# Optimization experiments

Hardware: AMD Instinct MI355X
Metric: run time of the kernel (lower is better)

The kernel has to match this reference:

```python
import jax, jax.numpy as jnp
import numpy as np

FIELD_NUM = 24

def _pair_indices(f):
    ii, jj = np.triu_indices(f, k=1)
    return jnp.asarray(ii), jnp.asarray(jj)

def setup_inputs() -> dict:
    key = jax.random.key(0)
    k1, k2 = jax.random.split(key)
    B, F, D = 16384, FIELD_NUM, 64
    P = F * (F - 1) // 2  # 276
    x = jax.random.normal(k1, (B, F, D), dtype=jnp.float32)
    W = jax.random.normal(k2, (P, D, D), dtype=jnp.float32) * 0.05
    return {"x": x, "W": W}

def reference(x, W):
    # x: (B, F, D) field embeddings; W: (P, D, D) per-pair bilinear matrices
    idx_i, idx_j = _pair_indices(FIELD_NUM)
    xi = x[:, idx_i, :]  # (B, P, D)
    xj = x[:, idx_j, :]  # (B, P, D)
    # sum_{p,d,e} xi[b,p,d] * W[p,d,e] * xj[b,p,e]
    logit = jnp.einsum('bpd,pde,bpe->b', xi, W, xj)
    return logit[:, None]  # (B, 1), matching tf output shape
```

## Files before the change

### kernel.cpp

```cpp
#include <hip/hip_runtime.h>
#include <stdint.h>

#define B_TOT 16384
#define F_NUM 24
#define D_DIM 64
#define P_NUM 276
#define BT    64
#define NTH   512
#define ROWS  770

typedef float f32x16 __attribute__((ext_vector_type(16)));
typedef short bf16x8 __attribute__((ext_vector_type(8)));

__device__ inline unsigned short f2bf(float f) {
    unsigned u = __float_as_uint(f);
    u += 0x7fffu + ((u >> 16) & 1u);
    return (unsigned short)(u >> 16);
}

struct WTab { int ent[8][36]; };
constexpr WTab build_tab() {
    WTab t{};
    const int fl[8][6] = {
        {0,12,-1,-1,-1,-1},
        {1,11,-1,-1,-1,-1},
        {2,10,-1,-1,-1,-1},
        {3, 9,-1,-1,-1,-1},
        {4, 8,-1,-1,-1,-1},
        {5, 7,-1,-1,-1,-1},
        {6,14,17,20,22,-1},
        {13,15,16,18,19,21}};
    for (int w = 0; w < 8; ++w) {
        int c = 0;
        for (int k = 0; k < 6; ++k) {
            int f = fl[w][k];
            if (f < 0) break;
            int base = 23 * f - f * (f - 1) / 2;
            for (int j = f + 1; j < 24; ++j)
                t.ent[w][c++] = (base + j - f - 1) | (j << 9) | (f << 14);
        }
        int last = t.ent[w][c - 1];
        while (c < 36) t.ent[w][c++] = last;
    }
    return t;
}
__device__ __constant__ WTab gtab = build_tab();

__global__ __launch_bounds__(256) void wprep(const float* __restrict__ W,
                                             unsigned short* __restrict__ afrag) {
    __shared__ __align__(16) unsigned short wlds[64 * 72];
    int p = blockIdx.x, t = threadIdx.x;
    const float4* src = (const float4*)(W + (size_t)p * 4096);
    #pragma unroll
    for (int c = 0; c < 4; ++c) {
        int i = t + c * 256;
        float4 v = src[i];
        int d = i >> 4;
        int e = (i & 15) * 4;
        ushort4 h; h.x=f2bf(v.x); h.y=f2bf(v.y); h.z=f2bf(v.z); h.w=f2bf(v.w);
        *(ushort4*)(&wlds[d * 72 + e]) = h;
    }
    __syncthreads();
    #pragma unroll
    for (int c = 0; c < 2; ++c) {
        int sl = t + c * 256;
        int u = sl >> 6, lane = sl & 63;
        int ks = u >> 1, m = u & 1;
        int d = m * 32 + (lane & 31);
        int e = ks * 16 + (lane >> 5) * 8;
        bf16x8 v = *(const bf16x8*)(&wlds[d * 72 + e]);
        size_t dst = ((size_t)((ks * P_NUM + p) * 2 + m) * 64 + lane) * 8;
        *(bf16x8*)(afrag + dst) = v;
    }
}

__global__ __launch_bounds__(NTH, 2) void fmfm_main(const float* __restrict__ x,
                                                    const unsigned short* __restrict__ afrag,
                                                    float* __restrict__ out) {
    __shared__ __align__(16) unsigned short xs[BT * ROWS];
    __shared__ float t_red[BT];
    const int tid = threadIdx.x;
    const int btile = blockIdx.x;
    const int lane = tid & 63;
    const int wv = __builtin_amdgcn_readfirstlane(tid >> 6);
    const int bcol = lane & 31;
    const int q = lane >> 5;

    if (tid < BT) t_red[tid] = 0.0f;

    const int cnt = (wv < 6) ? 34 : 36;
    const bf16x8* afr = (const bf16x8*)afrag;

    float tacc0 = 0.0f, tacc1 = 0.0f;
    f32x16 acc00, acc01, acc10, acc11;
    #pragma unroll
    for (int i = 0; i < 16; ++i) { acc00[i]=0.f; acc01[i]=0.f; acc10[i]=0.f; acc11[i]=0.f; }

    const float* xg  = x + (size_t)btile * BT * 1536;
    const float* xe0 = xg + (size_t)bcol * 1536 + 4 * q;
    const float* xe1 = xe0 + (size_t)32 * 1536;
    const unsigned short* xr0 = xs + bcol * ROWS;
    const unsigned short* xr1 = xs + (bcol + 32) * ROWS;

    for (int h = 0; h < 2; ++h) {
        __syncthreads();
        for (int k = 0; k < 24; ++k) {
            int g = tid + k * NTH;
            int row = g / 192;
            int r = g - row * 192;
            int f = r >> 3, i = r & 7;
            float4 v = *(const float4*)(xg + (size_t)row * 1536 + f * 64 + h * 32 + i * 4);
            ushort4 hh; hh.x=f2bf(v.x); hh.y=f2bf(v.y); hh.z=f2bf(v.z); hh.w=f2bf(v.w);
            *(ushort4*)(&xs[row * ROWS + f * 32 + i * 4]) = hh;
        }
        __syncthreads();

        const int ks0 = 2 * h;

        auto epi = [&](int f) {
            const float* e0 = xe0 + f * 64;
            const float* e1 = xe1 + f * 64;
            #pragma unroll
            for (int g = 0; g < 4; ++g) {
                float4 v = *(const float4*)(e0 + 8 * g);
                tacc0 += acc00[4*g+0]*v.x + acc00[4*g+1]*v.y + acc00[4*g+2]*v.z + acc00[4*g+3]*v.w;
                v = *(const float4*)(e0 + 32 + 8 * g);
                tacc0 += acc01[4*g+0]*v.x + acc01[4*g+1]*v.y + acc01[4*g+2]*v.z + acc01[4*g+3]*v.w;
                v = *(const float4*)(e1 + 8 * g);
                tacc1 += acc10[4*g+0]*v.x + acc10[4*g+1]*v.y + acc10[4*g+2]*v.z + acc10[4*g+3]*v.w;
                v = *(const float4*)(e1 + 32 + 8 * g);
                tacc1 += acc11[4*g+0]*v.x + acc11[4*g+1]*v.y + acc11[4*g+2]*v.z + acc11[4*g+3]*v.w;
            }
            #pragma unroll
            for (int i = 0; i < 16; ++i) { acc00[i]=0.f; acc01[i]=0.f; acc10[i]=0.f; acc11[i]=0.f; }
        };

        auto step = [&](int s, bf16x8* buf) {
            int e = gtab.ent[wv][s];
            int j = (e >> 9) & 31;
            int f = e >> 14;
            const unsigned short* a0 = xr0 + j * 32 + q * 8;
            const unsigned short* a1 = xr1 + j * 32 + q * 8;
            bf16x8 b00 = *(const bf16x8*)(a0);
            bf16x8 b01 = *(const bf16x8*)(a0 + 16);
            bf16x8 b10 = *(const bf16x8*)(a1);
            bf16x8 b11 = *(const bf16x8*)(a1 + 16);
            acc00 = __builtin_amdgcn_mfma_f32_32x32x16_bf16(buf[0], b00, acc00, 0, 0, 0);
            acc01 = __builtin_amdgcn_mfma_f32_32x32x16_bf16(buf[1], b00, acc01, 0, 0, 0);
            acc10 = __builtin_amdgcn_mfma_f32_32x32x16_bf16(buf[0], b10, acc10, 0, 0, 0);
            acc11 = __builtin_amdgcn_mfma_f32_32x32x16_bf16(buf[1], b10, acc11, 0, 0, 0);
            acc00 = __builtin_amdgcn_mfma_f32_32x32x16_bf16(buf[2], b01, acc00, 0, 0, 0);
            acc01 = __builtin_amdgcn_mfma_f32_32x32x16_bf16(buf[3], b01, acc01, 0, 0, 0);
            acc10 = __builtin_amdgcn_mfma_f32_32x32x16_bf16(buf[2], b11, acc10, 0, 0, 0);
            acc11 = __builtin_amdgcn_mfma_f32_32x32x16_bf16(buf[3], b11, acc11, 0, 0, 0);
            int sp = (s + 2 < cnt) ? s + 2 : cnt - 1;
            int pp = gtab.ent[wv][sp] & 511;
            #pragma unroll
            for (int u = 0; u < 4; ++u) {
                int ksl = u >> 1, m = u & 1;
                buf[u] = afr[(size_t)(((ks0 + ksl) * P_NUM + pp) * 2 + m) * 64 + lane];
            }
            if (j == 23) epi(f);
        };

        bf16x8 bufA[4], bufB[4];
        {
            int p0 = gtab.ent[wv][0] & 511;
            #pragma unroll
            for (int u = 0; u < 4; ++u) {
                int ksl = u >> 1, m = u & 1;
                bufA[u] = afr[(size_t)(((ks0 + ksl) * P_NUM + p0) * 2 + m) * 64 + lane];
            }
            int p1 = gtab.ent[wv][1] & 511;
            #pragma unroll
            for (int u = 0; u < 4; ++u) {
                int ksl = u >> 1, m = u & 1;
                bufB[u] = afr[(size_t)(((ks0 + ksl) * P_NUM + p1) * 2 + m) * 64 + lane];
            }
        }
        for (int s = 0; s < cnt; s += 2) {
            step(s,     bufA);
            step(s + 1, bufB);
        }
    }

    atomicAdd(&t_red[bcol],      tacc0);
    atomicAdd(&t_red[bcol + 32], tacc1);
    __syncthreads();
    if (tid < BT) out[(size_t)btile * BT + tid] = t_red[tid];
}

extern "C" void kernel_launch(void* const* d_in, const int* in_sizes, int n_in,
                              void* d_out, int out_size, void* d_ws, size_t ws_size,
                              hipStream_t stream) {
    const float* x = (const float*)d_in[0];
    const float* W = (const float*)d_in[1];
    float* out = (float*)d_out;
    unsigned short* afrag = (unsigned short*)d_ws;
    wprep<<<P_NUM, 256, 0, stream>>>(W, afrag);
    fmfm_main<<<B_TOT / BT, NTH, 0, stream>>>(x, afrag, out);
}
```

Baseline: 227.5 us.

## Stage x by field halves with full-depth K per pair instead of D halves

```diff
diff --git a/kernel.cpp b/kernel.cpp
--- a/kernel.cpp
+++ b/kernel.cpp
@@ -3,11 +3,10 @@
 
 #define B_TOT 16384
 #define F_NUM 24
-#define D_DIM 64
 #define P_NUM 276
 #define BT    64
 #define NTH   512
-#define ROWS  770
+#define ROWP  776
 
 typedef float f32x16 __attribute__((ext_vector_type(16)));
 typedef short bf16x8 __attribute__((ext_vector_type(8)));
@@ -18,33 +17,57 @@
     return (unsigned short)(u >> 16);
 }
 
-struct WTab { int ent[8][36]; };
-constexpr WTab build_tab() {
-    WTab t{};
-    const int fl[8][6] = {
-        {0,12,-1,-1,-1,-1},
-        {1,11,-1,-1,-1,-1},
-        {2,10,-1,-1,-1,-1},
-        {3, 9,-1,-1,-1,-1},
-        {4, 8,-1,-1,-1,-1},
-        {5, 7,-1,-1,-1,-1},
-        {6,14,17,20,22,-1},
-        {13,15,16,18,19,21}};
-    for (int w = 0; w < 8; ++w) {
-        int c = 0;
-        for (int k = 0; k < 6; ++k) {
-            int f = fl[w][k];
-            if (f < 0) break;
-            int base = 23 * f - f * (f - 1) / 2;
-            for (int j = f + 1; j < 24; ++j)
-                t.ent[w][c++] = (base + j - f - 1) | (j << 9) | (f << 14);
-        }
-        int last = t.ent[w][c - 1];
-        while (c < 36) t.ent[w][c++] = last;
+struct Tab { int ent[8][40]; int c1[8]; int c2[8]; };
+constexpr Tab build_tab() {
+    Tab t{};
+    int list[210][3] = {};
+    int n = 0;
+    for (int i = 0; i < 12; ++i)
+        for (int j = i + 1; j < 12; ++j) {
+            list[n][0] = 23 * i - i * (i - 1) / 2 + (j - i - 1);
+            list[n][1] = j;
+            list[n][2] = i;
+            ++n;
+        }
+    {
+        const int cnts[8] = {10, 8, 8, 8, 8, 8, 8, 8};
+        int pos = 0;
+        for (int w = 0; w < 8; ++w) {
+            t.c1[w] = cnts[w];
+            for (int k = 0; k < cnts[w]; ++k, ++pos) {
+                int flag = (k == cnts[w] - 1) ? 1
+                         : ((list[pos + 1][2] != list[pos][2]) ? 1 : 0);
+                t.ent[w][k] = list[pos][0] | (list[pos][1] << 9)
+                            | (list[pos][2] << 13) | (flag << 18);
+            }
+        }
+    }
+    n = 0;
+    for (int i = 0; i < 23; ++i) {
+        int j0 = (i < 12) ? 12 : i + 1;
+        for (int j = j0; j < 24; ++j) {
+            list[n][0] = 23 * i - i * (i - 1) / 2 + (j - i - 1);
+            list[n][1] = j - 12;
+            list[n][2] = i;
+            ++n;
+        }
+    }
+    {
+        const int cnts[8] = {26, 26, 26, 26, 26, 26, 26, 28};
+        int pos = 0;
+        for (int w = 0; w < 8; ++w) {
+            t.c2[w] = cnts[w];
+            for (int k = 0; k < cnts[w]; ++k, ++pos) {
+                int flag = (k == cnts[w] - 1) ? 1
+                         : ((list[pos + 1][2] != list[pos][2]) ? 1 : 0);
+                t.ent[w][t.c1[w] + k] = list[pos][0] | (list[pos][1] << 9)
+                                      | (list[pos][2] << 13) | (flag << 18);
+            }
+        }
     }
     return t;
 }
-__device__ __constant__ WTab gtab = build_tab();
+__device__ __constant__ Tab gtab = build_tab();
 
 __global__ __launch_bounds__(256) void wprep(const float* __restrict__ W,
                                              unsigned short* __restrict__ afrag) {
@@ -69,15 +92,14 @@
         int d = m * 32 + (lane & 31);
         int e = ks * 16 + (lane >> 5) * 8;
         bf16x8 v = *(const bf16x8*)(&wlds[d * 72 + e]);
-        size_t dst = ((size_t)((ks * P_NUM + p) * 2 + m) * 64 + lane) * 8;
-        *(bf16x8*)(afrag + dst) = v;
+        *(bf16x8*)(afrag + ((size_t)(p * 8 + u) * 64 + lane) * 8) = v;
     }
 }
 
 __global__ __launch_bounds__(NTH, 2) void fmfm_main(const float* __restrict__ x,
                                                     const unsigned short* __restrict__ afrag,
                                                     float* __restrict__ out) {
-    __shared__ __align__(16) unsigned short xs[BT * ROWS];
+    __shared__ __align__(16) unsigned short xs[BT * ROWP];
     __shared__ float t_red[BT];
     const int tid = threadIdx.x;
     const int btile = blockIdx.x;
@@ -85,102 +107,105 @@
     const int wv = __builtin_amdgcn_readfirstlane(tid >> 6);
     const int bcol = lane & 31;
     const int q = lane >> 5;
+    const int q8 = q * 8, q4 = q * 4;
 
     if (tid < BT) t_red[tid] = 0.0f;
 
-    const int cnt = (wv < 6) ? 34 : 36;
     const bf16x8* afr = (const bf16x8*)afrag;
-
-    float tacc0 = 0.0f, tacc1 = 0.0f;
-    f32x16 acc00, acc01, acc10, acc11;
+    const float* xg  = x + (size_t)btile * BT * 1536;
+    const float* xe0 = xg + (size_t)bcol * 1536 + q4;
+    const float* xe1 = xe0 + (size_t)32 * 1536;
+    const unsigned short* xr0 = xs + bcol * ROWP;
+    const unsigned short* xr1 = xs + (bcol + 32) * ROWP;
+
+    float tacc0 = 0.f, tacc1 = 0.f;
+    f32x16 a00, a01, a10, a11;
     #pragma unroll
-    for (int i = 0; i < 16; ++i) { acc00[i]=0.f; acc01[i]=0.f; acc10[i]=0.f; acc11[i]=0.f; }
-
-    const float* xg  = x + (size_t)btile * BT * 1536;
-    const float* xe0 = xg + (size_t)bcol * 1536 + 4 * q;
-    const float* xe1 = xe0 + (size_t)32 * 1536;
-    const unsigned short* xr0 = xs + bcol * ROWS;
-    const unsigned short* xr1 = xs + (bcol + 32) * ROWS;
-
-    for (int h = 0; h < 2; ++h) {
+    for (int i = 0; i < 16; ++i) { a00[i]=0.f; a01[i]=0.f; a10[i]=0.f; a11[i]=0.f; }
+
+    bf16x8 bufA[8], bufB[8];
+    auto lda = [&](int p, bf16x8* buf) {
+        const bf16x8* ap = afr + (size_t)p * 512 + lane;
+        #pragma unroll
+        for (int u = 0; u < 8; ++u) buf[u] = ap[u * 64];
+    };
+
+    auto epi = [&](int i) {
+        const float* e0 = xe0 + i * 64;
+        const float* e1 = xe1 + i * 64;
+        #pragma unroll
+        for (int g = 0; g < 4; ++g) {
+            float4 v = *(const float4*)(e0 + 8 * g);
+            tacc0 += a00[4*g+0]*v.x + a00[4*g+1]*v.y + a00[4*g+2]*v.z + a00[4*g+3]*v.w;
+            v = *(const float4*)(e0 + 32 + 8 * g);
+            tacc0 += a01[4*g+0]*v.x + a01[4*g+1]*v.y + a01[4*g+2]*v.z + a01[4*g+3]*v.w;
+            v = *(const float4*)(e1 + 8 * g);
+            tacc1 += a10[4*g+0]*v.x + a10[4*g+1]*v.y + a10[4*g+2]*v.z + a10[4*g+3]*v.w;
+            v = *(const float4*)(e1 + 32 + 8 * g);
+            tacc1 += a11[4*g+0]*v.x + a11[4*g+1]*v.y + a11[4*g+2]*v.z + a11[4*g+3]*v.w;
+        }
+        #pragma unroll
+        for (int k = 0; k < 16; ++k) { a00[k]=0.f; a01[k]=0.f; a10[k]=0.f; a11[k]=0.f; }
+    };
+
+    auto step = [&](int idx, int nxt, bf16x8* buf) {
+        int e = gtab.ent[wv][idx];
+        int jb = ((e >> 9) & 15) * 64 + q8;
+        int fi = (e >> 13) & 31;
+        const unsigned short* b0p = xr0 + jb;
+        const unsigned short* b1p = xr1 + jb;
+        bf16x8 b0k0 = *(const bf16x8*)(b0p);
+        bf16x8 b0k1 = *(const bf16x8*)(b0p + 16);
+        bf16x8 b0k2 = *(const bf16x8*)(b0p + 32);
+        bf16x8 b0k3 = *(const bf16x8*)(b0p + 48);
+        bf16x8 b1k0 = *(const bf16x8*)(b1p);
+        bf16x8 b1k1 = *(const bf16x8*)(b1p + 16);
+        bf16x8 b1k2 = *(const bf16x8*)(b1p + 32);
+        bf16x8 b1k3 = *(const bf16x8*)(b1p + 48);
+        a00 = __builtin_amdgcn_mfma_f32_32x32x16_bf16(buf[0], b0k0, a00, 0, 0, 0);
+        a01 = __builtin_amdgcn_mfma_f32_32x32x16_bf16(buf[1], b0k0, a01, 0, 0, 0);
+        a10 = __builtin_amdgcn_mfma_f32_32x32x16_bf16(buf[0], b1k0, a10, 0, 0, 0);
+        a11 = __builtin_amdgcn_mfma_f32_32x32x16_bf16(buf[1], b1k0, a11, 0, 0, 0);
+        a00 = __builtin_amdgcn_mfma_f32_32x32x16_bf16(buf[2], b0k1, a00, 0, 0, 0);
+        a01 = __builtin_amdgcn_mfma_f32_32x32x16_bf16(buf[3], b0k1, a01, 0, 0, 0);
+        a10 = __builtin_amdgcn_mfma_f32_32x32x16_bf16(buf[2], b1k1, a10, 0, 0, 0);
+        a11 = __builtin_amdgcn_mfma_f32_32x32x16_bf16(buf[3], b1k1, a11, 0, 0, 0);
+        a00 = __builtin_amdgcn_mfma_f32_32x32x16_bf16(buf[4], b0k2, a00, 0, 0, 0);
+        a01 = __builtin_amdgcn_mfma_f32_32x32x16_bf16(buf[5], b0k2, a01, 0, 0, 0);
+        a10 = __builtin_amdgcn_mfma_f32_32x32x16_bf16(buf[4], b1k2, a10, 0, 0, 0);
+        a11 = __builtin_amdgcn_mfma_f32_32x32x16_bf16(buf[5], b1k2, a11, 0, 0, 0);
+        a00 = __builtin_amdgcn_mfma_f32_32x32x16_bf16(buf[6], b0k3, a00, 0, 0, 0);
+        a01 = __builtin_amdgcn_mfma_f32_32x32x16_bf16(buf[7], b0k3, a01, 0, 0, 0);
+        a10 = __builtin_amdgcn_mfma_f32_32x32x16_bf16(buf[6], b1k3, a10, 0, 0, 0);
+        a11 = __builtin_amdgcn_mfma_f32_32x32x16_bf16(buf[7], b1k3, a11, 0, 0, 0);
+        lda(gtab.ent[wv][nxt] & 511, buf);
+        if (e & (1 << 18)) epi(fi);
+    };
+
+    #pragma unroll 1
+    for (int ph = 0; ph < 2; ++ph) {
+        int base = ph ? gtab.c1[wv] : 0;
+        int cnt  = ph ? gtab.c2[wv] : gtab.c1[wv];
+        lda(gtab.ent[wv][base] & 511, bufA);
+        lda(gtab.ent[wv][base + 1] & 511, bufB);
         __syncthreads();
-        for (int k = 0; k < 24; ++k) {
-            int g = tid + k * NTH;
-            int row = g / 192;
-            int r = g - row * 192;
-            int f = r >> 3, i = r & 7;
-            float4 v = *(const float4*)(xg + (size_t)row * 1536 + f * 64 + h * 32 + i * 4);
-            ushort4 hh; hh.x=f2bf(v.x); hh.y=f2bf(v.y); hh.z=f2bf(v.z); hh.w=f2bf(v.w);
-            *(ushort4*)(&xs[row * ROWS + f * 32 + i * 4]) = hh;
+        const float* src = xg + ph * 768;
+        #pragma unroll
+        for (int c = 0; c < 24; ++c) {
+            int idx = tid + c * NTH;
+            int row = idx / 192;
+            int c4  = idx - row * 192;
+            float4 v = *(const float4*)(src + (size_t)row * 1536 + c4 * 4);
+            ushort4 h; h.x=f2bf(v.x); h.y=f2bf(v.y); h.z=f2bf(v.z); h.w=f2bf(v.w);
+            *(ushort4*)(&xs[row * ROWP + c4 * 4]) = h;
         }
         __syncthreads();
-
-        const int ks0 = 2 * h;
-
-        auto epi = [&](int f) {
-            const float* e0 = xe0 + f * 64;
-            const float* e1 = xe1 + f * 64;
-            #pragma unroll
-            for (int g = 0; g < 4; ++g) {
-                float4 v = *(const float4*)(e0 + 8 * g);
-                tacc0 += acc00[4*g+0]*v.x + acc00[4*g+1]*v.y + acc00[4*g+2]*v.z + acc00[4*g+3]*v.w;
-                v = *(const float4*)(e0 + 32 + 8 * g);
-                tacc0 += acc01[4*g+0]*v.x + acc01[4*g+1]*v.y + acc01[4*g+2]*v.z + acc01[4*g+3]*v.w;
-                v = *(const float4*)(e1 + 8 * g);
-                tacc1 += acc10[4*g+0]*v.x + acc10[4*g+1]*v.y + acc10[4*g+2]*v.z + acc10[4*g+3]*v.w;
-                v = *(const float4*)(e1 + 32 + 8 * g);
-                tacc1 += acc11[4*g+0]*v.x + acc11[4*g+1]*v.y + acc11[4*g+2]*v.z + acc11[4*g+3]*v.w;
-            }
-            #pragma unroll
-            for (int i = 0; i < 16; ++i) { acc00[i]=0.f; acc01[i]=0.f; acc10[i]=0.f; acc11[i]=0.f; }
-        };
-
-        auto step = [&](int s, bf16x8* buf) {
-            int e = gtab.ent[wv][s];
-            int j = (e >> 9) & 31;
-            int f = e >> 14;
-            const unsigned short* a0 = xr0 + j * 32 + q * 8;
-            const unsigned short* a1 = xr1 + j * 32 + q * 8;
-            bf16x8 b00 = *(const bf16x8*)(a0);
-            bf16x8 b01 = *(const bf16x8*)(a0 + 16);
-            bf16x8 b10 = *(const bf16x8*)(a1);
-            bf16x8 b11 = *(const bf16x8*)(a1 + 16);
-            acc00 = __builtin_amdgcn_mfma_f32_32x32x16_bf16(buf[0], b00, acc00, 0, 0, 0);
-            acc01 = __builtin_amdgcn_mfma_f32_32x32x16_bf16(buf[1], b00, acc01, 0, 0, 0);
-            acc10 = __builtin_amdgcn_mfma_f32_32x32x16_bf16(buf[0], b10, acc10, 0, 0, 0);
-            acc11 = __builtin_amdgcn_mfma_f32_32x32x16_bf16(buf[1], b10, acc11, 0, 0, 0);
-            acc00 = __builtin_amdgcn_mfma_f32_32x32x16_bf16(buf[2], b01, acc00, 0, 0, 0);
-            acc01 = __builtin_amdgcn_mfma_f32_32x32x16_bf16(buf[3], b01, acc01, 0, 0, 0);
-            acc10 = __builtin_amdgcn_mfma_f32_32x32x16_bf16(buf[2], b11, acc10, 0, 0, 0);
-            acc11 = __builtin_amdgcn_mfma_f32_32x32x16_bf16(buf[3], b11, acc11, 0, 0, 0);
-            int sp = (s + 2 < cnt) ? s + 2 : cnt - 1;
-            int pp = gtab.ent[wv][sp] & 511;
-            #pragma unroll
-            for (int u = 0; u < 4; ++u) {
-                int ksl = u >> 1, m = u & 1;
-                buf[u] = afr[(size_t)(((ks0 + ksl) * P_NUM + pp) * 2 + m) * 64 + lane];
-            }
-            if (j == 23) epi(f);
-        };
-
-        bf16x8 bufA[4], bufB[4];
-        {
-            int p0 = gtab.ent[wv][0] & 511;
-            #pragma unroll
-            for (int u = 0; u < 4; ++u) {
-                int ksl = u >> 1, m = u & 1;
-                bufA[u] = afr[(size_t)(((ks0 + ksl) * P_NUM + p0) * 2 + m) * 64 + lane];
-            }
-            int p1 = gtab.ent[wv][1] & 511;
-            #pragma unroll
-            for (int u = 0; u < 4; ++u) {
-                int ksl = u >> 1, m = u & 1;
-                bufB[u] = afr[(size_t)(((ks0 + ksl) * P_NUM + p1) * 2 + m) * 64 + lane];
-            }
-        }
-        for (int s = 0; s < cnt; s += 2) {
-            step(s,     bufA);
-            step(s + 1, bufB);
+        int end = base + cnt;
+        for (int s = base; s < end; s += 2) {
+            int n0 = (s + 2 < end) ? s + 2 : end - 1;
+            int n1 = (s + 3 < end) ? s + 3 : end - 1;
+            step(s,     n0, bufA);
+            step(s + 1, n1, bufB);
         }
     }
 
```

After: 225.9 us. Within noise of the previous version (-0.7%).
